# Kernel tuning notes

Hardware: AMD Instinct MI355X
Metric: run time of the kernel (lower is better)

Reference implementation:

```python
import jax, jax.numpy as jnp
import numpy as np

N = 20000   # nodes
E = 320000  # edges (before self-loops)
F_IN = 128  # in_feats
H = 4       # heads
C = 64      # hidden (per-head channels; concat=False averages heads)
G = 64      # graphs in batch
EPS = 1e-5  # BatchNorm eps


def _gat(x, src, dst, W, a_src, a_dst, bias):
    # PyG GATConv, concat=False: project, per-edge LeakyReLU attention,
    # segment-softmax over destination nodes, scatter-add, mean over heads.
    h = (x @ W).reshape(N, H, C)                    # [N,H,C]
    es = (h * a_src).sum(-1)                        # [N,H]
    ed = (h * a_dst).sum(-1)                        # [N,H]
    e = jax.nn.leaky_relu(es[src] + ed[dst], 0.2)   # [Etot,H]
    m = jax.ops.segment_max(e, dst, num_segments=N)
    m = jnp.where(jnp.isfinite(m), m, 0.0)          # nodes with no in-edges
    p = jnp.exp(e - m[dst])
    s = jax.ops.segment_sum(p, dst, num_segments=N)
    alpha = p / (s[dst] + 1e-16)                    # PyG softmax epsilon
    out = jax.ops.segment_sum(h[src] * alpha[:, :, None], dst, num_segments=N)
    return out.mean(axis=1) + bias                  # [N,C]


def _bn(x, g, b):
    # BatchNorm1d in training mode: biased batch statistics over nodes
    mu = x.mean(axis=0)
    var = ((x - mu) ** 2).mean(axis=0)
    return (x - mu) * jax.lax.rsqrt(var + EPS) * g + b


def setup_inputs() -> dict:
    key = jax.random.key(0)
    ks = jax.random.split(key, 16)
    x = jax.random.normal(ks[0], (N, F_IN), dtype=jnp.float32)
    edge_index = jax.random.randint(ks[1], (2, E), 0, N, dtype=jnp.int32)
    batch_idx = jnp.sort(jax.random.randint(ks[2], (N,), 0, G, dtype=jnp.int32))
    s1 = 1.0 / np.sqrt(F_IN)
    s2 = 1.0 / np.sqrt(C)
    return {
        "x": x,
        "W1": jax.random.normal(ks[3], (F_IN, H * C), jnp.float32) * s1,
        "a_src1": jax.random.normal(ks[4], (H, C), jnp.float32) * s2,
        "a_dst1": jax.random.normal(ks[5], (H, C), jnp.float32) * s2,
        "b1": jnp.zeros((C,), jnp.float32),
        "Wskip": jax.random.normal(ks[6], (F_IN, C), jnp.float32) * s1,
        "bskip": jnp.zeros((C,), jnp.float32),
        "g1": jnp.ones((C,), jnp.float32),
        "be1": jnp.zeros((C,), jnp.float32),
        "W2": jax.random.normal(ks[7], (C, H * C), jnp.float32) * s2,
        "a_src2": jax.random.normal(ks[8], (H, C), jnp.float32) * s2,
        "a_dst2": jax.random.normal(ks[9], (H, C), jnp.float32) * s2,
        "b2": jnp.zeros((C,), jnp.float32),
        "g2": jnp.ones((C,), jnp.float32),
        "be2": jnp.zeros((C,), jnp.float32),
        "edge_index": edge_index,
        "batch_idx": batch_idx,
    }


def reference(x, W1, a_src1, a_dst1, b1, Wskip, bskip, g1, be1,
              W2, a_src2, a_dst2, b2, g2, be2, edge_index, batch_idx):
    # add self-loops (PyG GATConv default add_self_loops=True)
    loop = jnp.arange(N, dtype=edge_index.dtype)
    src = jnp.concatenate([edge_index[0], loop])
    dst = jnp.concatenate([edge_index[1], loop])

    x0 = x
    h = _gat(x, src, dst, W1, a_src1, a_dst1, b1)
    h = jax.nn.gelu(_bn(h, g1, be1) + x0 @ Wskip + bskip, approximate=False)
    # dropout is identity in eval mode
    h2 = _gat(h, src, dst, W2, a_src2, a_dst2, b2)
    h2 = jax.nn.gelu(_bn(h2, g2, be2) + h, approximate=False)

    # global mean pool over graphs
    sums = jax.ops.segment_sum(h2, batch_idx, num_segments=G)
    cnts = jax.ops.segment_sum(jnp.ones((N,), h2.dtype), batch_idx, num_segments=G)
    return sums / jnp.maximum(cnts, 1.0)[:, None]
```

## Files before the change

kernel.cpp:

```cpp
#include <hip/hip_runtime.h>
#include <math.h>

#define NN   20000
#define EE   320000
#define ETOT 340000
#define FIN  128
#define HH   4
#define CC   64
#define HC   256
#define GG   64
#define BN_EPS 1e-5f
#define S1   384
#define S2   320
#define NBUCK 64

typedef _Float16 v8h __attribute__((ext_vector_type(8)));
typedef float    v4f __attribute__((ext_vector_type(4)));

__device__ __forceinline__ unsigned short f2bf(float f) {
    unsigned u = __float_as_uint(f);
    unsigned r = (u + 0x7FFF + ((u >> 16) & 1)) >> 16;
    return (unsigned short)r;
}
__device__ __forceinline__ float bf2f(unsigned short u) {
    return __uint_as_float((unsigned)u << 16);
}
__device__ __forceinline__ float gelu_exact(float v) {
    return 0.5f * v * (1.f + erff(v * 0.70710678118654752f));
}

__global__ __launch_bounds__(256) void pre1_kernel(
        const int* __restrict__ bidx, int* __restrict__ gstart,
        const float* __restrict__ W1, const float* __restrict__ Wskip,
        const float* __restrict__ W2,
        const float* __restrict__ as1, const float* __restrict__ ad1,
        const float* __restrict__ as2, const float* __restrict__ ad2,
        _Float16* __restrict__ BT1, _Float16* __restrict__ BT2,
        const int* __restrict__ ei, int* __restrict__ deg, int* __restrict__ epos,
        float* __restrict__ outz) {
    int b = blockIdx.x, t = threadIdx.x;
    if (b < 79) {
        int i = b * 256 + t;
        if (i >= NN) return;
        int cur = bidx[i];
        if (i == 0) { for (int g = 0; g <= cur; ++g) gstart[g] = 0; }
        else { int prev = bidx[i - 1]; for (int g = prev + 1; g <= cur; ++g) gstart[g] = i; }
        if (i == NN - 1) { for (int g = cur + 1; g <= GG; ++g) gstart[g] = NN; }
    } else if (b < 271) {
        int i = (b - 79) * 256 + t;
        int col = i >> 7, k = i & 127;
        float v;
        if (col < 256) {
            v = W1[k * 256 + (col & 3) * 64 + (col >> 2)];
        } else if (col < 320) {
            v = Wskip[k * 64 + (col - 256)];
        } else if (col < 328) {
            int kk = col - 320, h = kk & 3;
            const float* av = (kk < 4 ? as1 : ad1) + h * 64;
            const float* wr = W1 + k * 256 + h * 64;
            float s = 0.f;
            #pragma unroll 8
            for (int c = 0; c < 64; ++c) s += wr[c] * av[c];
            v = s;
        } else v = 0.f;
        BT1[i] = (_Float16)v;
    } else if (b < 351) {
        int i = (b - 271) * 256 + t;
        int col = i >> 6, k = i & 63;
        float v;
        if (col < 256) {
            v = W2[k * 256 + (col & 3) * 64 + (col >> 2)];
        } else if (col < 264) {
            int kk = col - 256, h = kk & 3;
            const float* av = (kk < 4 ? as2 : ad2) + h * 64;
            const float* wr = W2 + k * 256 + h * 64;
            float s = 0.f;
            #pragma unroll 8
            for (int c = 0; c < 64; ++c) s += wr[c] * av[c];
            v = s;
        } else v = 0.f;
        BT2[i] = (_Float16)v;
    } else if (b < 1680) {
        int i = (b - 351) * 256 + t;
        if (i >= ETOT) return;
        int d = (i < EE) ? ei[EE + i] : (i - EE);
        epos[i] = atomicAdd(&deg[d], 1);
    } else {
        int i = (b - 1680) * 256 + t;
        outz[i] = 0.f;
    }
}

__global__ void fill_kernel(const int* __restrict__ ei, const int* __restrict__ off,
        const int* __restrict__ epos, int* __restrict__ csr_src) {
    int i = blockIdx.x * 256 + threadIdx.x;
    if (i >= ETOT) return;
    int s, d;
    if (i < EE) { s = ei[i]; d = ei[EE + i]; } else { s = i - EE; d = i - EE; }
    csr_src[off[d] + epos[i]] = s;
}

template<int NCB>
__global__ __launch_bounds__(256) void gemm_mfma(const float* __restrict__ A,
        const _Float16* __restrict__ BT, int M, int K,
        unsigned short* __restrict__ h4b, float* __restrict__ skipO,
        float* __restrict__ esf, float* __restrict__ edf,
        int escol0, int do_scan,
        const int* __restrict__ deg, int* __restrict__ off) {
    int b = blockIdx.x;
    int t = threadIdx.x;
    if (do_scan && b == 626) {
        const int CH = 79;
        __shared__ int bs[256];
        int base = t * CH;
        int sum = 0;
        for (int j = 0; j < CH; ++j) {
            int i = base + j;
            sum += (i < NN) ? deg[i] : 0;
        }
        bs[t] = sum; __syncthreads();
        for (int s = 1; s < 256; s <<= 1) {
            int x = (t >= s) ? bs[t - s] : 0;
            __syncthreads(); bs[t] += x; __syncthreads();
        }
        int run = (t == 0) ? 0 : bs[t - 1];
        for (int j = 0; j < CH; ++j) {
            int i = base + j;
            if (i < NN) { off[i] = run; run += deg[i]; }
        }
        if (t == 255) off[NN] = ETOT;
        return;
    }
    const int COLT = 2 * NCB * 16;
    __shared__ _Float16 sA[64][40];
    __shared__ _Float16 sBT[2 * NCB * 16][40];
    int tile = b & 1;
    int col0 = tile * COLT;
    int row0 = (b >> 1) * 64;
    int wave = t >> 6, lane = t & 63;
    int l15 = lane & 15, quad = lane >> 4;
    int rb0 = (wave >> 1) * 2;
    int cb0 = (wave & 1) * NCB;
    v4f acc[2][NCB] = {};
    for (int k0 = 0; k0 < K; k0 += 32) {
        {
            int r = t >> 2, c8 = t & 3;
            int gr = row0 + r;
            float4 v0 = make_float4(0.f, 0.f, 0.f, 0.f);
            float4 v1 = make_float4(0.f, 0.f, 0.f, 0.f);
            if (gr < M) {
                v0 = *(const float4*)&A[(size_t)gr * K + k0 + c8 * 8];
                v1 = *(const float4*)&A[(size_t)gr * K + k0 + c8 * 8 + 4];
            }
            v8h hv;
            hv[0] = (_Float16)v0.x; hv[1] = (_Float16)v0.y;
            hv[2] = (_Float16)v0.z; hv[3] = (_Float16)v0.w;
            hv[4] = (_Float16)v1.x; hv[5] = (_Float16)v1.y;
            hv[6] = (_Float16)v1.z; hv[7] = (_Float16)v1.w;
            *(v8h*)&sA[r][c8 * 8] = hv;
        }
        for (int j = t; j < COLT * 4; j += 256) {
            int c = j >> 2, s = j & 3;
            *(v8h*)&sBT[c][s * 8] = *(const v8h*)&BT[(size_t)(col0 + c) * K + k0 + s * 8];
        }
        __syncthreads();
        v8h af0 = *(const v8h*)&sA[(rb0 + 0) * 16 + l15][quad * 8];
        v8h af1 = *(const v8h*)&sA[(rb0 + 1) * 16 + l15][quad * 8];
        #pragma unroll
        for (int c = 0; c < NCB; ++c) {
            v8h bf = *(const v8h*)&sBT[(cb0 + c) * 16 + l15][quad * 8];
            acc[0][c] = __builtin_amdgcn_mfma_f32_16x16x32_f16(af0, bf, acc[0][c], 0, 0, 0);
            acc[1][c] = __builtin_amdgcn_mfma_f32_16x16x32_f16(af1, bf, acc[1][c], 0, 0, 0);
        }
        __syncthreads();
    }
    #pragma unroll
    for (int rr = 0; rr < 2; ++rr) {
        #pragma unroll
        for (int c = 0; c < NCB; ++c) {
            int gcol = col0 + (cb0 + c) * 16 + l15;
            #pragma unroll
            for (int reg = 0; reg < 4; ++reg) {
                int gr = row0 + (rb0 + rr) * 16 + quad * 4 + reg;
                if (gr >= M) continue;
                float v = acc[rr][c][reg];
                if (gcol < 256) {
                    h4b[(size_t)gr * HC + gcol] = f2bf(v);
                } else if (skipO != nullptr && gcol < 320) {
                    skipO[(size_t)gr * CC + (gcol - 256)] = v;
                } else if (gcol >= escol0 && gcol < escol0 + 8) {
                    if (gcol < escol0 + 4) esf[gr * 4 + (gcol - escol0)] = v;
                    else                   edf[gr * 4 + (gcol - escol0 - 4)] = v;
                }
            }
        }
    }
}

__device__ __forceinline__ void edge_acc(const float4 esv, const ushort4 hv,
        const float4 edn, float4& acc, float4& ssum) {
    float e0 = esv.x + edn.x; e0 = fmaxf(e0, 0.2f * e0); float w0 = __expf(e0);
    float e1 = esv.y + edn.y; e1 = fmaxf(e1, 0.2f * e1); float w1 = __expf(e1);
    float e2 = esv.z + edn.z; e2 = fmaxf(e2, 0.2f * e2); float w2 = __expf(e2);
    float e3 = esv.w + edn.w; e3 = fmaxf(e3, 0.2f * e3); float w3 = __expf(e3);
    acc.x += w0 * bf2f(hv.x); ssum.x += w0;
    acc.y += w1 * bf2f(hv.y); ssum.y += w1;
    acc.z += w2 * bf2f(hv.z); ssum.z += w2;
    acc.w += w3 * bf2f(hv.w); ssum.w += w3;
}

__global__ __launch_bounds__(256) void aggr_kernel(const unsigned short* __restrict__ h4b,
        const float4* __restrict__ es4, const float4* __restrict__ ed4,
        const int* __restrict__ off, const int* __restrict__ csr_src,
        const float* __restrict__ bias, float* __restrict__ out,
        float* __restrict__ sbuck) {
    int wave = threadIdx.x >> 6, lane = threadIdx.x & 63;
    int n = blockIdx.x * 4 + wave;
    float4 edn = ed4[n];
    float4 acc = make_float4(0.f, 0.f, 0.f, 0.f);
    float4 ssum = make_float4(0.f, 0.f, 0.f, 0.f);
    int beg = off[n], end = off[n + 1];
    int j = beg;
    for (; j + 4 <= end; j += 4) {
        int s0 = csr_src[j + 0];
        int s1 = csr_src[j + 1];
        int s2 = csr_src[j + 2];
        int s3 = csr_src[j + 3];
        float4 E0 = es4[s0];
        float4 E1 = es4[s1];
        float4 E2 = es4[s2];
        float4 E3 = es4[s3];
        ushort4 v0 = *(const ushort4*)&h4b[(size_t)s0 * HC + lane * 4];
        ushort4 v1 = *(const ushort4*)&h4b[(size_t)s1 * HC + lane * 4];
        ushort4 v2 = *(const ushort4*)&h4b[(size_t)s2 * HC + lane * 4];
        ushort4 v3 = *(const ushort4*)&h4b[(size_t)s3 * HC + lane * 4];
        edge_acc(E0, v0, edn, acc, ssum);
        edge_acc(E1, v1, edn, acc, ssum);
        edge_acc(E2, v2, edn, acc, ssum);
        edge_acc(E3, v3, edn, acc, ssum);
    }
    for (; j < end; ++j) {
        int s = csr_src[j];
        float4 E = es4[s];
        ushort4 v = *(const ushort4*)&h4b[(size_t)s * HC + lane * 4];
        edge_acc(E, v, edn, acc, ssum);
    }
    float val = 0.25f * (acc.x / (ssum.x + 1e-16f) + acc.y / (ssum.y + 1e-16f) +
                         acc.z / (ssum.z + 1e-16f) + acc.w / (ssum.w + 1e-16f)) + bias[lane];
    out[n * CC + lane] = val;
    __shared__ float ls[4][64], lq[4][64];
    ls[wave][lane] = val;
    lq[wave][lane] = val * val;
    __syncthreads();
    if (wave == 0) {
        float s = ls[0][lane] + ls[1][lane] + ls[2][lane] + ls[3][lane];
        float q = lq[0][lane] + lq[1][lane] + lq[2][lane] + lq[3][lane];
        int bk = (blockIdx.x & (NBUCK - 1)) * 128;
        atomicAdd(&sbuck[bk + lane], s);
        atomicAdd(&sbuck[bk + 64 + lane], q);
    }
}

__global__ __launch_bounds__(256) void bnapply1_kernel(const float* __restrict__ gout,
        const float* __restrict__ sbuck, const float* __restrict__ g,
        const float* __restrict__ be, const float* __restrict__ skip,
        const float* __restrict__ bskip, float* __restrict__ outm) {
    __shared__ float tmp[128];
    __shared__ float smu[64], sinv[64];
    int t = threadIdx.x;
    if (t < 128) {
        float s = 0.f;
        #pragma unroll 16
        for (int k = 0; k < NBUCK; ++k) s += sbuck[k * 128 + t];
        tmp[t] = s;
    }
    __syncthreads();
    if (t < 64) {
        float mu  = tmp[t] * (1.f / NN);
        float var = tmp[64 + t] * (1.f / NN) - mu * mu;
        smu[t] = mu;
        sinv[t] = rsqrtf(var + BN_EPS) * g[t];
    }
    __syncthreads();
    int i = blockIdx.x * 256 + t;
    int ch = i & 63;
    float v = (gout[i] - smu[ch]) * sinv[ch] + be[ch] + skip[i] + bskip[ch];
    outm[i] = gelu_exact(v);
}

__global__ __launch_bounds__(256) void bnapply2_kernel(const float* __restrict__ gout,
        const float* __restrict__ sbuck, const float* __restrict__ g,
        const float* __restrict__ be, const float* __restrict__ resid,
        const int* __restrict__ bidx, const int* __restrict__ gstart,
        float* __restrict__ out) {
    __shared__ float tmp[128];
    __shared__ float smu[64], sinv[64];
    __shared__ float ls[4][64];
    __shared__ int gi[4];
    int t = threadIdx.x;
    if (t < 128) {
        float s = 0.f;
        #pragma unroll 16
        for (int k = 0; k < NBUCK; ++k) s += sbuck[k * 128 + t];
        tmp[t] = s;
    }
    __syncthreads();
    if (t < 64) {
        float mu  = tmp[t] * (1.f / NN);
        float var = tmp[64 + t] * (1.f / NN) - mu * mu;
        smu[t] = mu;
        sinv[t] = rsqrtf(var + BN_EPS) * g[t];
    }
    __syncthreads();
    int i = blockIdx.x * 256 + t;
    int ch = i & 63;
    int wave = t >> 6;
    int n = i >> 6;
    float v = (gout[i] - smu[ch]) * sinv[ch] + be[ch] + resid[i];
    v = gelu_exact(v);
    int gg = bidx[n];
    int cnt = gstart[gg + 1] - gstart[gg];
    ls[wave][ch] = v * (1.f / (float)cnt);
    if (ch == 0) gi[wave] = gg;
    __syncthreads();
    if (wave == 0) {
        if (gi[0] == gi[1] && gi[1] == gi[2] && gi[2] == gi[3]) {
            float s = ls[0][ch] + ls[1][ch] + ls[2][ch] + ls[3][ch];
            atomicAdd(&out[gi[0] * CC + ch], s);
        } else {
            #pragma unroll
            for (int w2 = 0; w2 < 4; ++w2)
                atomicAdd(&out[gi[w2] * CC + ch], ls[w2][ch]);
        }
    }
}

extern "C" void kernel_launch(void* const* d_in, const int* in_sizes, int n_in,
                              void* d_out, int out_size, void* d_ws, size_t ws_size,
                              hipStream_t stream) {
    const float* x      = (const float*)d_in[0];
    const float* W1     = (const float*)d_in[1];
    const float* a_src1 = (const float*)d_in[2];
    const float* a_dst1 = (const float*)d_in[3];
    const float* b1     = (const float*)d_in[4];
    const float* Wskip  = (const float*)d_in[5];
    const float* bskip  = (const float*)d_in[6];
    const float* g1     = (const float*)d_in[7];
    const float* be1    = (const float*)d_in[8];
    const float* W2     = (const float*)d_in[9];
    const float* a_src2 = (const float*)d_in[10];
    const float* a_dst2 = (const float*)d_in[11];
    const float* b2     = (const float*)d_in[12];
    const float* g2     = (const float*)d_in[13];
    const float* be2    = (const float*)d_in[14];
    const int*   ei     = (const int*)d_in[15];
    const int*   bidx   = (const int*)d_in[16];
    float* out = (float*)d_out;

    char* w = (char*)d_ws;
    size_t o = 0;
    auto alloc = [&](size_t bytes) -> void* {
        void* p = w + o;
        o = (o + bytes + 255) & ~(size_t)255;
        return p;
    };

    unsigned short* h4b = (unsigned short*)alloc((size_t)NN * HC * 2);
    float4* es4 = (float4*)alloc((size_t)NN * 16);
    float4* ed4 = (float4*)alloc((size_t)NN * 16);
    float* skip = (float*)alloc((size_t)NN * CC * 4);
    float* gout = (float*)alloc((size_t)NN * CC * 4);
    float* hmid = (float*)alloc((size_t)NN * CC * 4);
    _Float16* BT1 = (_Float16*)alloc((size_t)S1 * FIN * 2);
    _Float16* BT2 = (_Float16*)alloc((size_t)S2 * CC * 2);
    int* off    = (int*)alloc((size_t)(NN + 1) * 4);
    int* csr    = (int*)alloc((size_t)ETOT * 4);
    int* epos   = (int*)alloc((size_t)ETOT * 4);
    int* gstart = (int*)alloc((size_t)(GG + 1) * 4);
    char* zbase = w + o;
    int* deg      = (int*)alloc((size_t)NN * 4);
    float* sbuck1 = (float*)alloc((size_t)NBUCK * 128 * 4);
    float* sbuck2 = (float*)alloc((size_t)NBUCK * 128 * 4);
    size_t zbytes = (size_t)((w + o) - zbase);

    hipMemsetAsync(zbase, 0, zbytes, stream);

    int ebk = (ETOT + 255) / 256;
    int nodeblk = NN / 4;

    pre1_kernel<<<79 + 192 + 80 + ebk + 16, 256, 0, stream>>>(bidx, gstart,
            W1, Wskip, W2, a_src1, a_dst1, a_src2, a_dst2, BT1, BT2, ei, deg, epos,
            out);

    gemm_mfma<6><<<627, 256, 0, stream>>>(x, BT1, NN, FIN,
            h4b, skip, (float*)es4, (float*)ed4, 320, 1, deg, off);
    fill_kernel<<<ebk, 256, 0, stream>>>(ei, off, epos, csr);
    aggr_kernel<<<nodeblk, 256, 0, stream>>>(h4b, es4, ed4, off, csr, b1, gout,
            sbuck1);
    bnapply1_kernel<<<NN * CC / 256, 256, 0, stream>>>(
        gout, sbuck1, g1, be1, skip, bskip, hmid);

    gemm_mfma<5><<<626, 256, 0, stream>>>(hmid, BT2, NN, CC,
            h4b, (float*)nullptr, (float*)es4, (float*)ed4, 256, 0,
            (const int*)nullptr, (int*)nullptr);
    aggr_kernel<<<nodeblk, 256, 0, stream>>>(h4b, es4, ed4, off, csr, b2, gout,
            sbuck2);
    bnapply2_kernel<<<NN * CC / 256, 256, 0, stream>>>(
        gout, sbuck2, g2, be2, hmid, bidx, gstart, out);
}
```

Measured before the change: 249.1 us.

## Fuse layer-1 BatchNorm+GELU into layer-2 GEMM prologue and unroll aggregation by 8

Removes the separate bnapply1 kernel. The second-layer MFMA GEMM now reduces the BN bucket statistics itself, applies BN, skip add and GELU while loading its A tile, and writes hmid from one of the two column tiles. This saves a launch and one full read/write pass over the intermediate activations. The cost is that both column-tile blocks recompute the GELU and every block re-reduces the 64 buckets. Separately, the aggregation loop gains an 8-way unrolled gather stage to put more loads in flight.

```diff
diff --git a/kernel.cpp b/kernel.cpp
--- a/kernel.cpp
+++ b/kernel.cpp
@@ -197,6 +197,111 @@
     }
 }
 
+template<int NCB>
+__global__ __launch_bounds__(256) void gemm_mfma_bn(const float* __restrict__ gout,
+        const float* __restrict__ skip, const float* __restrict__ sbuck,
+        const float* __restrict__ g, const float* __restrict__ be,
+        const float* __restrict__ bskip, float* __restrict__ hmid,
+        const _Float16* __restrict__ BT, int M, int K,
+        unsigned short* __restrict__ h4b,
+        float* __restrict__ esf, float* __restrict__ edf, int escol0) {
+    const int COLT = 2 * NCB * 16;
+    __shared__ _Float16 sA[64][40];
+    __shared__ _Float16 sBT[2 * NCB * 16][40];
+    __shared__ float tmp[128];
+    __shared__ float sscale[64], sshift[64];
+    int t = threadIdx.x;
+    int b = blockIdx.x;
+    if (t < 128) {
+        float s = 0.f;
+        #pragma unroll 16
+        for (int k = 0; k < NBUCK; ++k) s += sbuck[k * 128 + t];
+        tmp[t] = s;
+    }
+    __syncthreads();
+    if (t < 64) {
+        float mu  = tmp[t] * (1.f / NN);
+        float var = tmp[64 + t] * (1.f / NN) - mu * mu;
+        float inv = rsqrtf(var + BN_EPS) * g[t];
+        sscale[t] = inv;
+        sshift[t] = be[t] + bskip[t] - mu * inv;
+    }
+    __syncthreads();
+    int tile = b & 1;
+    int col0 = tile * COLT;
+    int row0 = (b >> 1) * 64;
+    int wave = t >> 6, lane = t & 63;
+    int l15 = lane & 15, quad = lane >> 4;
+    int rb0 = (wave >> 1) * 2;
+    int cb0 = (wave & 1) * NCB;
+    v4f acc[2][NCB] = {};
+    for (int k0 = 0; k0 < K; k0 += 32) {
+        {
+            int r = t >> 2, c8 = t & 3;
+            int gr = row0 + r;
+            int cb = k0 + c8 * 8;
+            float vv[8];
+            if (gr < M) {
+                float4 q0 = *(const float4*)&gout[(size_t)gr * CC + cb];
+                float4 q1 = *(const float4*)&gout[(size_t)gr * CC + cb + 4];
+                float4 p0 = *(const float4*)&skip[(size_t)gr * CC + cb];
+                float4 p1 = *(const float4*)&skip[(size_t)gr * CC + cb + 4];
+                float qa[8] = {q0.x,q0.y,q0.z,q0.w,q1.x,q1.y,q1.z,q1.w};
+                float pa[8] = {p0.x,p0.y,p0.z,p0.w,p1.x,p1.y,p1.z,p1.w};
+                #pragma unroll
+                for (int u = 0; u < 8; ++u)
+                    vv[u] = gelu_exact(qa[u] * sscale[cb + u] + sshift[cb + u] + pa[u]);
+                if (tile == 0) {
+                    float4 w0 = make_float4(vv[0], vv[1], vv[2], vv[3]);
+                    float4 w1 = make_float4(vv[4], vv[5], vv[6], vv[7]);
+                    *(float4*)&hmid[(size_t)gr * CC + cb] = w0;
+                    *(float4*)&hmid[(size_t)gr * CC + cb + 4] = w1;
+                }
+            } else {
+                #pragma unroll
+                for (int u = 0; u < 8; ++u) vv[u] = 0.f;
+            }
+            v8h hv;
+            #pragma unroll
+            for (int u = 0; u < 8; ++u) hv[u] = (_Float16)vv[u];
+            *(v8h*)&sA[r][c8 * 8] = hv;
+        }
+        for (int j = t; j < COLT * 4; j += 256) {
+            int c = j >> 2, s = j & 3;
+            *(v8h*)&sBT[c][s * 8] = *(const v8h*)&BT[(size_t)(col0 + c) * K + k0 + s * 8];
+        }
+        __syncthreads();
+        v8h af0 = *(const v8h*)&sA[(rb0 + 0) * 16 + l15][quad * 8];
+        v8h af1 = *(const v8h*)&sA[(rb0 + 1) * 16 + l15][quad * 8];
+        #pragma unroll
+        for (int c = 0; c < NCB; ++c) {
+            v8h bf = *(const v8h*)&sBT[(cb0 + c) * 16 + l15][quad * 8];
+            acc[0][c] = __builtin_amdgcn_mfma_f32_16x16x32_f16(af0, bf, acc[0][c], 0, 0, 0);
+            acc[1][c] = __builtin_amdgcn_mfma_f32_16x16x32_f16(af1, bf, acc[1][c], 0, 0, 0);
+        }
+        __syncthreads();
+    }
+    #pragma unroll
+    for (int rr = 0; rr < 2; ++rr) {
+        #pragma unroll
+        for (int c = 0; c < NCB; ++c) {
+            int gcol = col0 + (cb0 + c) * 16 + l15;
+            #pragma unroll
+            for (int reg = 0; reg < 4; ++reg) {
+                int gr = row0 + (rb0 + rr) * 16 + quad * 4 + reg;
+                if (gr >= M) continue;
+                float v = acc[rr][c][reg];
+                if (gcol < 256) {
+                    h4b[(size_t)gr * HC + gcol] = f2bf(v);
+                } else if (gcol >= escol0 && gcol < escol0 + 8) {
+                    if (gcol < escol0 + 4) esf[gr * 4 + (gcol - escol0)] = v;
+                    else                   edf[gr * 4 + (gcol - escol0 - 4)] = v;
+                }
+            }
+        }
+    }
+}
+
 __device__ __forceinline__ void edge_acc(const float4 esv, const ushort4 hv,
         const float4 edn, float4& acc, float4& ssum) {
     float e0 = esv.x + edn.x; e0 = fmaxf(e0, 0.2f * e0); float w0 = __expf(e0);
@@ -221,6 +326,20 @@
     float4 ssum = make_float4(0.f, 0.f, 0.f, 0.f);
     int beg = off[n], end = off[n + 1];
     int j = beg;
+    for (; j + 8 <= end; j += 8) {
+        int s[8];
+        #pragma unroll
+        for (int u = 0; u < 8; ++u) s[u] = csr_src[j + u];
+        float4 E[8];
+        #pragma unroll
+        for (int u = 0; u < 8; ++u) E[u] = es4[s[u]];
+        ushort4 v[8];
+        #pragma unroll
+        for (int u = 0; u < 8; ++u)
+            v[u] = *(const ushort4*)&h4b[(size_t)s[u] * HC + lane * 4];
+        #pragma unroll
+        for (int u = 0; u < 8; ++u) edge_acc(E[u], v[u], edn, acc, ssum);
+    }
     for (; j + 4 <= end; j += 4) {
         int s0 = csr_src[j + 0];
         int s1 = csr_src[j + 1];
@@ -259,33 +378,6 @@
         atomicAdd(&sbuck[bk + lane], s);
         atomicAdd(&sbuck[bk + 64 + lane], q);
     }
-}
-
-__global__ __launch_bounds__(256) void bnapply1_kernel(const float* __restrict__ gout,
-        const float* __restrict__ sbuck, const float* __restrict__ g,
-        const float* __restrict__ be, const float* __restrict__ skip,
-        const float* __restrict__ bskip, float* __restrict__ outm) {
-    __shared__ float tmp[128];
-    __shared__ float smu[64], sinv[64];
-    int t = threadIdx.x;
-    if (t < 128) {
-        float s = 0.f;
-        #pragma unroll 16
-        for (int k = 0; k < NBUCK; ++k) s += sbuck[k * 128 + t];
-        tmp[t] = s;
-    }
-    __syncthreads();
-    if (t < 64) {
-        float mu  = tmp[t] * (1.f / NN);
-        float var = tmp[64 + t] * (1.f / NN) - mu * mu;
-        smu[t] = mu;
-        sinv[t] = rsqrtf(var + BN_EPS) * g[t];
-    }
-    __syncthreads();
-    int i = blockIdx.x * 256 + t;
-    int ch = i & 63;
-    float v = (gout[i] - smu[ch]) * sinv[ch] + be[ch] + skip[i] + bskip[ch];
-    outm[i] = gelu_exact(v);
 }
 
 __global__ __launch_bounds__(256) void bnapply2_kernel(const float* __restrict__ gout,
@@ -397,12 +489,9 @@
     fill_kernel<<<ebk, 256, 0, stream>>>(ei, off, epos, csr);
     aggr_kernel<<<nodeblk, 256, 0, stream>>>(h4b, es4, ed4, off, csr, b1, gout,
             sbuck1);
-    bnapply1_kernel<<<NN * CC / 256, 256, 0, stream>>>(
-        gout, sbuck1, g1, be1, skip, bskip, hmid);
-
-    gemm_mfma<5><<<626, 256, 0, stream>>>(hmid, BT2, NN, CC,
-            h4b, (float*)nullptr, (float*)es4, (float*)ed4, 256, 0,
-            (const int*)nullptr, (int*)nullptr);
+
+    gemm_mfma_bn<5><<<626, 256, 0, stream>>>(gout, skip, sbuck1, g1, be1, bskip,
+            hmid, BT2, NN, CC, h4b, (float*)es4, (float*)ed4, 256);
     aggr_kernel<<<nodeblk, 256, 0, stream>>>(h4b, es4, ed4, off, csr, b2, gout,
             sbuck2);
     bnapply2_kernel<<<NN * CC / 256, 256, 0, stream>>>(
```

Result: slower. 257.0 us (+3.2%).
